# Performance work log

Measured on AMD Instinct MI355X. Metric: run time of the kernel, lower is better.

Reference implementation:

```python
import jax, jax.numpy as jnp
import numpy as np

EMBED = 1024
HEADS = 16
DEPTH = EMBED // HEADS
FFN_DIM = 4096
EPS = 1e-9


def layer_norm(x, g, b):
    mu = jnp.mean(x, axis=-1, keepdims=True)
    var = jnp.mean(jnp.square(x - mu), axis=-1, keepdims=True)
    return (x - mu) * jax.lax.rsqrt(var + EPS) * g + b


def setup_inputs() -> dict:
    key = jax.random.key(0)
    ks = jax.random.split(key, 16)
    B, S = 2, 2048
    s_e = 1.0 / np.sqrt(EMBED)
    s_f = 1.0 / np.sqrt(FFN_DIM)
    return {
        "x": jax.random.normal(ks[0], (B, S, EMBED), dtype=jnp.float32),
        "mask": jnp.zeros((B, 1, 1, S), dtype=jnp.float32),
        "wq_w": jax.random.normal(ks[1], (EMBED, EMBED), dtype=jnp.float32) * s_e,
        "wq_b": jnp.zeros((EMBED,), dtype=jnp.float32),
        "wk_w": jax.random.normal(ks[2], (EMBED, EMBED), dtype=jnp.float32) * s_e,
        "wk_b": jnp.zeros((EMBED,), dtype=jnp.float32),
        "wv_w": jax.random.normal(ks[3], (EMBED, EMBED), dtype=jnp.float32) * s_e,
        "wv_b": jnp.zeros((EMBED,), dtype=jnp.float32),
        "wo_w": jax.random.normal(ks[4], (EMBED, EMBED), dtype=jnp.float32) * s_e,
        "wo_b": jnp.zeros((EMBED,), dtype=jnp.float32),
        "f1_w": jax.random.normal(ks[5], (EMBED, FFN_DIM), dtype=jnp.float32) * s_e,
        "f1_b": jnp.zeros((FFN_DIM,), dtype=jnp.float32),
        "f2_w": jax.random.normal(ks[6], (FFN_DIM, EMBED), dtype=jnp.float32) * s_f,
        "f2_b": jnp.zeros((EMBED,), dtype=jnp.float32),
        "ln1_g": jnp.ones((EMBED,), dtype=jnp.float32),
        "ln1_b": jnp.zeros((EMBED,), dtype=jnp.float32),
        "ln2_g": jnp.ones((EMBED,), dtype=jnp.float32),
        "ln2_b": jnp.zeros((EMBED,), dtype=jnp.float32),
    }


def reference(x, mask, wq_w, wq_b, wk_w, wk_b, wv_w, wv_b, wo_w, wo_b,
              f1_w, f1_b, f2_w, f2_b, ln1_g, ln1_b, ln2_g, ln2_b):
    B, S, E = x.shape

    def split_heads(t):  # (B,S,E) -> (B,H,S,D)
        return t.reshape(B, S, HEADS, DEPTH).transpose(0, 2, 1, 3)

    q = split_heads(x @ wq_w + wq_b)
    k = split_heads(x @ wk_w + wk_b)
    v = split_heads(x @ wv_w + wv_b)

    logits = jnp.einsum("bhqd,bhkd->bhqk", q, k) / jnp.sqrt(jnp.float32(DEPTH))
    logits = logits + mask * -1e12  # mask broadcast (B,1,1,S)
    attn = jax.nn.softmax(logits, axis=-1)
    out = jnp.einsum("bhqk,bhkd->bhqd", attn, v)
    out = out.transpose(0, 2, 1, 3).reshape(B, S, E)
    out = out @ wo_w + wo_b

    # dropout is identity (is_train=False)
    h = layer_norm(out + x, ln1_g, ln1_b)
    f = jax.nn.relu(h @ f1_w + f1_b) @ f2_w + f2_b
    return layer_norm(f + h, ln2_g, ln2_b)
```

## Files before the change

kernel.cpp:

```cpp
#include <hip/hip_runtime.h>
#include <hip/hip_bf16.h>
#include <stdint.h>

typedef __hip_bfloat16 bf16;
typedef __attribute__((ext_vector_type(8))) short short8;
typedef __attribute__((ext_vector_type(4))) short short4v;
typedef __attribute__((ext_vector_type(4))) float floatx4;

#define E_DIM 1024
#define S_LEN 2048
#define NB    2
#define NH    16
#define HD    64
#define FFN   4096
#define MTOT  4096

__device__ __forceinline__ void gl_lds16(const void* g, void* l) {
  __builtin_amdgcn_global_load_lds(
      (__attribute__((address_space(1))) void*)(g),
      (__attribute__((address_space(3))) void*)(l), 16, 0, 0);
}

#define VMW(N)  do { asm volatile("s_waitcnt vmcnt(" #N ")" ::: "memory"); \
                     __builtin_amdgcn_sched_barrier(0); } while (0)
#define LGKM0   do { asm volatile("s_waitcnt lgkmcnt(0)" ::: "memory"); } while (0)
#define BARR    do { asm volatile("s_barrier" ::: "memory"); } while (0)

__device__ __forceinline__ int fswz_v(int row) { return row & 7; }
__device__ __forceinline__ int fswz_k(int row) {
  return ((row ^ (row >> 3)) & 3) | ((((row >> 3) ^ (row >> 4)) & 1) << 2);
}

__device__ __forceinline__ float bf16bits2float(short s) {
  union { unsigned u; float f; } c;
  c.u = ((unsigned)(unsigned short)s) << 16;
  return c.f;
}

__global__ __launch_bounds__(256)
void cvt_bf16(const float* __restrict__ in, bf16* __restrict__ out) {
  const size_t i = ((size_t)blockIdx.x * 256 + threadIdx.x) * 4;
  float4 v = *(const float4*)(in + i);
  out[i + 0] = __float2bfloat16(v.x);
  out[i + 1] = __float2bfloat16(v.y);
  out[i + 2] = __float2bfloat16(v.z);
  out[i + 3] = __float2bfloat16(v.w);
}

__global__ __launch_bounds__(256)
void transpose_all(const float* __restrict__ wq, const float* __restrict__ wk,
                   const float* __restrict__ wv, const float* __restrict__ wo,
                   const float* __restrict__ f1, const float* __restrict__ f2,
                   bf16* __restrict__ W3T, bf16* __restrict__ woT,
                   bf16* __restrict__ f1T, bf16* __restrict__ f2T) {
  const int z = blockIdx.z;
  const float* in;
  bf16* out;
  int inStride, outStride, rOff, cOff;
  if (z < 4) {
    in = (z == 0) ? wq : (z == 1) ? wk : (z == 2) ? wv : wo;
    out = (z < 3) ? (W3T + (size_t)z * 1024 * 1024) : woT;
    inStride = 1024; outStride = 1024; rOff = 0; cOff = 0;
  } else if (z < 8) {
    in = f1; out = f1T; inStride = 4096; outStride = 1024;
    rOff = 0; cOff = (z - 4) * 1024;
  } else {
    in = f2; out = f2T; inStride = 1024; outStride = 4096;
    rOff = (z - 8) * 1024; cOff = 0;
  }
  __shared__ float tile[32][33];
  const int tx = threadIdx.x & 31;
  const int ty = threadIdx.x >> 5;
  const int c0 = blockIdx.x * 32;
  const int r0 = blockIdx.y * 32;
#pragma unroll
  for (int j = 0; j < 32; j += 8)
    tile[ty + j][tx] =
        in[(size_t)(rOff + r0 + ty + j) * inStride + cOff + c0 + tx];
  __syncthreads();
#pragma unroll
  for (int j = 0; j < 32; j += 8)
    out[(size_t)(cOff + c0 + ty + j) * outStride + rOff + r0 + tx] =
        __float2bfloat16(tile[tx][ty + j]);
}

__global__ __launch_bounds__(256)
void prep_bias(const float* __restrict__ qb, const float* __restrict__ kb,
               const float* __restrict__ vb, float* __restrict__ out) {
  const int i = blockIdx.x * 256 + threadIdx.x;
  float v = (i < 1024) ? qb[i] * 0.125f
                       : ((i < 2048) ? kb[i - 1024] : vb[i - 2048]);
  out[i] = v;
}

__global__ __launch_bounds__(512, 2)
void gemm256(const bf16* __restrict__ A, const bf16* __restrict__ B,
             const float* __restrict__ bias, void* __restrict__ Cout,
             void* __restrict__ Cout2,
             int M, int N, int Kpart, int lda, int mode) {
  __shared__ alignas(16) bf16 sA[2][2][128 * 64];
  __shared__ alignas(16) bf16 sB[2][2][128 * 64];
  const int tid   = threadIdx.x;
  const int wave  = tid >> 6;
  const int lane  = tid & 63;
  const int row16 = lane & 15;
  const int quad  = lane >> 4;
  const int sw7   = row16 & 7;

  const int gx = gridDim.x;
  const int nwg = gx * gridDim.y;
  const int cpx = nwg >> 3;
  int id = blockIdx.y * gx + blockIdx.x;
  id = (id & 7) * cpx + (id >> 3);
  const int m0 = (id % gx) * 256;
  const int n0 = (id / gx) * 256;

  const int wm2 = wave >> 2;
  const int wn4 = wave & 3;
  const int wm  = wm2 * 128;
  const int wn  = wn4 * 64;
  const int hB  = wn4 >> 1;
  const int rbB = (wn4 & 1) * 64;
  const int koff = blockIdx.z * Kpart;
  const int NS = Kpart >> 6;

  floatx4 acc[8][4];
#pragma unroll
  for (int i = 0; i < 8; i++)
#pragma unroll
    for (int j = 0; j < 4; j++) {
      floatx4 z = {0.f, 0.f, 0.f, 0.f};
      acc[i][j] = z;
    }

  auto stage_half = [&](const bf16* G, int rowBase, int k0, bf16* dst) {
#pragma unroll
    for (int j = 0; j < 2; ++j) {
      const int r = wave * 16 + j * 8 + (lane >> 3);
      const int g = (lane & 7) ^ (r & 7);
      gl_lds16(G + (size_t)(rowBase + r) * lda + k0 + g * 8,
               dst + (wave * 16 + j * 8) * 64);
    }
  };

  short8 aF[8][2];
  short8 bF[4][2];
  const bf16* aH = nullptr;
  const bf16* bH = nullptr;

  auto read_aF = [&](int mi0) {
#pragma unroll
    for (int mi = 0; mi < 4; ++mi)
#pragma unroll
      for (int kk = 0; kk < 2; ++kk)
        aF[mi0 + mi][kk] = *(const short8*)(
            aH + ((mi0 + mi) * 16 + row16) * 64 + (((kk * 4 + quad) ^ sw7) << 3));
  };
  auto read_bF = [&](int ni0) {
#pragma unroll
    for (int ni = 0; ni < 2; ++ni)
#pragma unroll
      for (int kk = 0; kk < 2; ++kk)
        bF[ni0 + ni][kk] = *(const short8*)(
            bH + (rbB + (ni0 + ni) * 16 + row16) * 64 + (((kk * 4 + quad) ^ sw7) << 3));
  };
  auto qmf = [&](int mi0, int ni0) {
    __builtin_amdgcn_s_setprio(1);
#pragma unroll
    for (int mi = 0; mi < 4; ++mi)
#pragma unroll
      for (int ni = 0; ni < 2; ++ni)
#pragma unroll
        for (int kk = 0; kk < 2; ++kk)
          acc[mi0 + mi][ni0 + ni] = __builtin_amdgcn_mfma_f32_16x16x32_bf16(
              aF[mi0 + mi][kk], bF[ni0 + ni][kk], acc[mi0 + mi][ni0 + ni], 0, 0, 0);
    __builtin_amdgcn_s_setprio(0);
  };

  stage_half(A, m0,       koff,      &sA[0][0][0]);
  stage_half(A, m0 + 128, koff,      &sA[0][1][0]);
  stage_half(B, n0,       koff,      &sB[0][0][0]);
  stage_half(B, n0 + 128, koff,      &sB[0][1][0]);
  stage_half(A, m0,       koff + 64, &sA[1][0][0]);
  stage_half(A, m0 + 128, koff + 64, &sA[1][1][0]);

  for (int s = 0; s < NS; ++s) {
    const int b = s & 1;
    aH = &sA[b][wm2][0];
    bH = &sB[b][hB][0];
    if (s + 1 < NS) VMW(4); else VMW(0);
    BARR;
    if (s + 1 < NS) {
      const int kn1 = koff + (s + 1) * 64;
      stage_half(B, n0,       kn1, &sB[b ^ 1][0][0]);
      stage_half(B, n0 + 128, kn1, &sB[b ^ 1][1][0]);
    }
    read_aF(0);
    read_bF(0);
    read_aF(4);
    qmf(0, 0);
    qmf(4, 0);
    LGKM0;
    BARR;
    if (s + 2 < NS) {
      const int kn2 = koff + (s + 2) * 64;
      stage_half(A, m0,       kn2, &sA[b][0][0]);
      stage_half(A, m0 + 128, kn2, &sA[b][1][0]);
    }
    read_bF(2);
    qmf(0, 2);
    qmf(4, 2);
  }

  float bval[4] = {0.f, 0.f, 0.f, 0.f};
  if (mode != 0) {
#pragma unroll
    for (int ni = 0; ni < 4; ni++) bval[ni] = bias[n0 + wn + ni * 16 + row16];
  }

#pragma unroll
  for (int mi = 0; mi < 8; mi++) {
#pragma unroll
    for (int ni = 0; ni < 4; ni++) {
      const int col = n0 + wn + ni * 16 + row16;
      if (mode == 0) {
        float* co = (float*)((blockIdx.z < 2) ? Cout : Cout2) +
                    (size_t)(blockIdx.z & 1) * M * N;
#pragma unroll
        for (int r = 0; r < 4; r++) {
          const int row = m0 + wm + mi * 16 + quad * 4 + r;
          co[(size_t)row * N + col] = acc[mi][ni][r];
        }
      } else if (mode == 1) {
#pragma unroll
        for (int r = 0; r < 4; r++) {
          const int row = m0 + wm + mi * 16 + quad * 4 + r;
          float v = acc[mi][ni][r] + bval[ni];
          v = v > 0.f ? v : 0.f;
          ((bf16*)Cout)[(size_t)row * N + col] = __float2bfloat16(v);
        }
      } else {
        const int mat = col >> 10;
        const int c10 = col & 1023;
        const int hh = c10 >> 6, dd = c10 & 63;
        const float scl = (mat == 0) ? 0.125f : 1.0f;
        bf16* qout = (bf16*)Cout;
        const int rbase = m0 + wm + mi * 16 + quad * 4;
        const int b2 = rbase >> 11, ss = rbase & 2047;
        const size_t bh = (size_t)b2 * NH + hh;
        if (mat == 2) {
          bf16* vt = qout + (1 << 23);
          short4v pv;
#pragma unroll
          for (int r = 0; r < 4; r++) {
            bf16 t = __float2bfloat16(acc[mi][ni][r] + bval[ni]);
            pv[r] = *(short*)&t;
          }
          *(short4v*)(vt + (bh * HD + dd) * S_LEN + ss) = pv;
        } else {
          bf16* o = (mat == 1) ? (qout + (1 << 22)) : qout;
#pragma unroll
          for (int r = 0; r < 4; r++) {
            float v = acc[mi][ni][r] * scl + bval[ni];
            o[(bh * S_LEN + ss + r) * HD + dd] = __float2bfloat16(v);
          }
        }
      }
    }
  }
}

__global__ __launch_bounds__(256, 4)
void flash_attn(const bf16* __restrict__ Q, const bf16* __restrict__ K,
                const bf16* __restrict__ Vt, const float* __restrict__ mask,
                bf16* __restrict__ Out) {
  __shared__ alignas(16) bf16 sK[2][64 * 64];
  __shared__ alignas(16) bf16 sV[2][64 * 64];
  __shared__ alignas(16) float sM[S_LEN];

  const int tid   = threadIdx.x;
  const int wave  = tid >> 6;
  const int lane  = tid & 63;
  const int row16 = lane & 15;
  const int quad  = lane >> 4;
  const int bh = blockIdx.y;
  const int b = bh >> 4, h = bh & 15;
  const int q0 = blockIdx.x * 64;
  const int qg = q0 + wave * 16 + row16;

  const bf16* qp = Q + ((size_t)bh * S_LEN + qg) * HD;
  short8 qf0 = *(const short8*)(qp + quad * 8);
  short8 qf1 = *(const short8*)(qp + 32 + quad * 8);

  for (int i = tid; i < S_LEN / 4; i += 256) {
    float4 mv = ((const float4*)(mask + (size_t)b * S_LEN))[i];
    float4 w = {-1e12f * mv.x, -1e12f * mv.y, -1e12f * mv.z, -1e12f * mv.w};
    ((float4*)sM)[i] = w;
  }
  LGKM0;

  float lsum = 0.f;
  floatx4 ov[4];
#pragma unroll
  for (int i = 0; i < 4; i++) { floatx4 z = {0.f,0.f,0.f,0.f}; ov[i] = z; }

  const bf16* Kbase = K + (size_t)bh * S_LEN * HD;
  const bf16* Vbase = Vt + (size_t)bh * HD * S_LEN;
  const int NT = S_LEN / 64;

  auto stage = [&](int kt) {
    const bf16* Kg = Kbase + (size_t)kt * 64 * HD;
    const bf16* Vg = Vbase + kt * 64;
    bf16* dK = sK[kt & 1];
    bf16* dV = sV[kt & 1];
#pragma unroll
    for (int j = 0; j < 2; ++j) {
      const int ch = wave * 2 + j;
      const int row = ch * 8 + (lane >> 3);
      const int sc_ = lane & 7;
      gl_lds16(Kg + row * 64 + ((sc_ ^ fswz_k(row)) * 8), dK + ch * 512);
      gl_lds16(Vg + (size_t)row * S_LEN + ((sc_ ^ fswz_v(row)) * 8), dV + ch * 512);
    }
  };

  stage(0);

  for (int kt = 0; kt < NT; ++kt) {
    if (kt + 1 < NT) {
      stage(kt + 1);
      VMW(4);
    } else {
      VMW(0);
    }
    BARR;

    const bf16* Kb = sK[kt & 1];
    const bf16* Vb = sV[kt & 1];

    floatx4 sc[4];
#pragma unroll
    for (int mi = 0; mi < 4; mi++) {
      const int row = ((row16 >> 2) << 3) + (row16 & 3) + ((mi & 1) << 2) + ((mi >> 1) << 5);
      const int fk = fswz_k(row);
      short8 kf0 = *(const short8*)(Kb + row * 64 + ((quad ^ fk) << 3));
      short8 kf1 = *(const short8*)(Kb + row * 64 + (((4 + quad) ^ fk) << 3));
      floatx4 z = {0.f, 0.f, 0.f, 0.f};
      z = __builtin_amdgcn_mfma_f32_16x16x32_bf16(kf0, qf0, z, 0, 0, 0);
      sc[mi] = __builtin_amdgcn_mfma_f32_16x16x32_bf16(kf1, qf1, z, 0, 0, 0);
    }

#pragma unroll
    for (int mi = 0; mi < 4; mi++) {
      float4 mv = *(const float4*)(sM + kt * 64 + (quad << 3) + ((mi & 1) << 2) + ((mi >> 1) << 5));
      sc[mi][0] = __expf(sc[mi][0] + mv.x);
      sc[mi][1] = __expf(sc[mi][1] + mv.y);
      sc[mi][2] = __expf(sc[mi][2] + mv.z);
      sc[mi][3] = __expf(sc[mi][3] + mv.w);
      lsum += sc[mi][0] + sc[mi][1] + sc[mi][2] + sc[mi][3];
    }

    short8 pf[2];
#pragma unroll
    for (int ks = 0; ks < 2; ks++)
#pragma unroll
      for (int jp = 0; jp < 4; jp++) {
        const int mi = 2 * ks + (jp >> 1);
        const int r0 = (jp & 1) * 2;
        bf16 p0 = __float2bfloat16(sc[mi][r0]);
        bf16 p1 = __float2bfloat16(sc[mi][r0 + 1]);
        pf[ks][2 * jp]     = *(short*)&p0;
        pf[ks][2 * jp + 1] = *(short*)&p1;
      }

#pragma unroll
    for (int mi = 0; mi < 4; mi++) {
      const int row = mi * 16 + row16;
      const int fv = fswz_v(row);
      short8 v0 = *(const short8*)(Vb + row * 64 + ((quad ^ fv) << 3));
      short8 v1 = *(const short8*)(Vb + row * 64 + (((4 + quad) ^ fv) << 3));
      ov[mi] = __builtin_amdgcn_mfma_f32_16x16x32_bf16(v0, pf[0], ov[mi], 0, 0, 0);
      ov[mi] = __builtin_amdgcn_mfma_f32_16x16x32_bf16(v1, pf[1], ov[mi], 0, 0, 0);
    }
    BARR;
  }

  lsum += __shfl_xor(lsum, 16);
  lsum += __shfl_xor(lsum, 32);
  const float inv = 1.0f / lsum;
#pragma unroll
  for (int mi = 0; mi < 4; mi++) {
    short4v pv;
#pragma unroll
    for (int r = 0; r < 4; r++) {
      bf16 t = __float2bfloat16(ov[mi][r] * inv);
      pv[r] = *(short*)&t;
    }
    *(short4v*)(Out + ((size_t)(b * S_LEN + qg)) * E_DIM + h * HD + mi * 16 + quad * 4) = pv;
  }
}

__global__ __launch_bounds__(256)
void ln_reduce(const float* __restrict__ p0, const float* __restrict__ p1,
               const float* __restrict__ p2, const float* __restrict__ p3,
               const float* __restrict__ resf, const bf16* __restrict__ resb,
               const float* __restrict__ bias, const float* __restrict__ g,
               const float* __restrict__ be, float* __restrict__ outf,
               bf16* __restrict__ outb) {
  const int row = blockIdx.x;
  const int tid = threadIdx.x;
  const size_t base = (size_t)row * 1024;
  const int c = tid * 4;
  float4 a = *(const float4*)(p0 + base + c);
  float4 bq = *(const float4*)(p1 + base + c);
  float4 xv;
  xv.x = a.x + bq.x;
  xv.y = a.y + bq.y;
  xv.z = a.z + bq.z;
  xv.w = a.w + bq.w;
  if (p2) {
    float4 a2 = *(const float4*)(p2 + base + c);
    float4 a3 = *(const float4*)(p3 + base + c);
    xv.x += a2.x + a3.x;
    xv.y += a2.y + a3.y;
    xv.z += a2.z + a3.z;
    xv.w += a2.w + a3.w;
  }
  float4 rv;
  if (resf) {
    rv = *(const float4*)(resf + base + c);
  } else {
    short4v rb = *(const short4v*)((const short*)resb + base + c);
    rv.x = bf16bits2float(rb[0]);
    rv.y = bf16bits2float(rb[1]);
    rv.z = bf16bits2float(rb[2]);
    rv.w = bf16bits2float(rb[3]);
  }
  float4 bi = *(const float4*)(bias + c);
  xv.x += rv.x + bi.x;
  xv.y += rv.y + bi.y;
  xv.z += rv.z + bi.z;
  xv.w += rv.w + bi.w;
  float s  = xv.x + xv.y + xv.z + xv.w;
  float s2 = xv.x * xv.x + xv.y * xv.y + xv.z * xv.z + xv.w * xv.w;
#pragma unroll
  for (int d = 1; d < 64; d <<= 1) {
    s  += __shfl_xor(s, d);
    s2 += __shfl_xor(s2, d);
  }
  __shared__ float red[2][4];
  const int wave = tid >> 6;
  if ((tid & 63) == 0) { red[0][wave] = s; red[1][wave] = s2; }
  __syncthreads();
  s  = red[0][0] + red[0][1] + red[0][2] + red[0][3];
  s2 = red[1][0] + red[1][1] + red[1][2] + red[1][3];
  const float mu  = s * (1.0f / 1024.0f);
  const float var = s2 * (1.0f / 1024.0f) - mu * mu;
  const float rs  = rsqrtf(var + 1e-9f);
  float4 gg = *(const float4*)(g + c);
  float4 bb = *(const float4*)(be + c);
  float4 y;
  y.x = (xv.x - mu) * rs * gg.x + bb.x;
  y.y = (xv.y - mu) * rs * gg.y + bb.y;
  y.z = (xv.z - mu) * rs * gg.z + bb.z;
  y.w = (xv.w - mu) * rs * gg.w + bb.w;
  if (outf) *(float4*)(outf + base + c) = y;
  if (outb) {
    bf16* o = outb + base + c;
    o[0] = __float2bfloat16(y.x);
    o[1] = __float2bfloat16(y.y);
    o[2] = __float2bfloat16(y.z);
    o[3] = __float2bfloat16(y.w);
  }
}

extern "C" void kernel_launch(void* const* d_in, const int* in_sizes, int n_in,
                              void* d_out, int out_size, void* d_ws,
                              size_t ws_size, hipStream_t stream) {
  const float* x    = (const float*)d_in[0];
  const float* mask = (const float*)d_in[1];
  const float* wq_w = (const float*)d_in[2];
  const float* wq_b = (const float*)d_in[3];
  const float* wk_w = (const float*)d_in[4];
  const float* wk_b = (const float*)d_in[5];
  const float* wv_w = (const float*)d_in[6];
  const float* wv_b = (const float*)d_in[7];
  const float* wo_w = (const float*)d_in[8];
  const float* wo_b = (const float*)d_in[9];
  const float* f1_w = (const float*)d_in[10];
  const float* f1_b = (const float*)d_in[11];
  const float* f2_w = (const float*)d_in[12];
  const float* f2_b = (const float*)d_in[13];
  const float* ln1_g = (const float*)d_in[14];
  const float* ln1_b = (const float*)d_in[15];
  const float* ln2_g = (const float*)d_in[16];
  const float* ln2_b = (const float*)d_in[17];
  float* out = (float*)d_out;

  char* ws = (char*)d_ws;
  const size_t MB = 1u << 20;
  bf16*  xbf   = (bf16*)(ws + 0 * MB);
  bf16*  W3T   = (bf16*)(ws + 8 * MB);
  bf16*  woT   = (bf16*)(ws + 14 * MB);
  float* bqkv  = (float*)(ws + 16 * MB);
  bf16*  Qb    = (bf16*)(ws + 17 * MB);
  bf16*  attnb = (bf16*)(ws + 0 * MB);
  bf16*  ffn1  = (bf16*)(ws + 17 * MB);
  bf16*  f1T   = (bf16*)(ws + 49 * MB);
  bf16*  f2T   = (bf16*)(ws + 57 * MB);
  float* P01   = (float*)(ws + 65 * MB);
  bf16*  hbf   = (bf16*)(ws + 97 * MB);
  float* P23   = (float*)(ws + 105 * MB);
  const size_t PS = (size_t)MTOT * E_DIM;

  const int KS = (ws_size >= (size_t)137 * MB) ? 4 : 2;
  const float* p2 = (KS == 4) ? P23 : nullptr;
  const float* p3 = (KS == 4) ? P23 + PS : nullptr;

  cvt_bf16<<<4096, 256, 0, stream>>>(x, xbf);
  transpose_all<<<dim3(32, 32, 12), 256, 0, stream>>>(
      wq_w, wk_w, wv_w, wo_w, f1_w, f2_w, W3T, woT, f1T, f2T);
  prep_bias<<<12, 256, 0, stream>>>(wq_b, wk_b, wv_b, bqkv);

  gemm256<<<dim3(16, 12, 1), 512, 0, stream>>>(
      xbf, W3T, bqkv, Qb, nullptr, MTOT, 3 * E_DIM, E_DIM, E_DIM, 2);

  flash_attn<<<dim3(S_LEN / 64, NB * NH), 256, 0, stream>>>(
      Qb, Qb + (1 << 22), Qb + (1 << 23), mask, attnb);

  gemm256<<<dim3(16, 4, KS), 512, 0, stream>>>(
      attnb, woT, nullptr, P01, P23, MTOT, E_DIM, E_DIM / KS, E_DIM, 0);

  ln_reduce<<<MTOT, 256, 0, stream>>>(P01, P01 + PS, p2, p3, x, nullptr,
                                      wo_b, ln1_g, ln1_b, nullptr, hbf);

  gemm256<<<dim3(16, 16, 1), 512, 0, stream>>>(
      hbf, f1T, f1_b, ffn1, nullptr, MTOT, FFN, E_DIM, E_DIM, 1);

  gemm256<<<dim3(16, 4, KS), 512, 0, stream>>>(
      ffn1, f2T, nullptr, P01, P23, MTOT, E_DIM, FFN / KS, FFN, 0);

  ln_reduce<<<MTOT, 256, 0, stream>>>(P01, P01 + PS, p2, p3, nullptr, hbf,
                                      f2_b, ln2_g, ln2_b, out, nullptr);
}
```

Before: 377.4 us.

## Fold log2e into Q scale, use exp2, compute row sums via MFMA

Folds log2(e) into the query scale and the mask constant so the softmax can use the raw v_exp_f32 (exp2) instruction in place of __expf. It replaces the per-lane scalar row-sum accumulation and cross-lane shuffles with two MFMAs against a ones vector, so the sum comes out of the matrix unit. The sum now uses bf16-rounded probabilities, consistent with what feeds P·V. Separately, the GEMM main loop reorders its fragment reads and MFMA calls to issue all B reads first and overlap the A reads with compute.

Measured after the change: 376.0 us. Within noise of the previous version (-0.4%).

```diff
diff --git a/kernel.cpp b/kernel.cpp
--- a/kernel.cpp
+++ b/kernel.cpp
@@ -15,6 +15,9 @@
 #define FFN   4096
 #define MTOT  4096
 
+#define QSCALE 0.18033688011112042f
+#define MSCALE -1.4426950408889634e12f
+
 __device__ __forceinline__ void gl_lds16(const void* g, void* l) {
   __builtin_amdgcn_global_load_lds(
       (__attribute__((address_space(1))) void*)(g),
@@ -25,6 +28,12 @@
                      __builtin_amdgcn_sched_barrier(0); } while (0)
 #define LGKM0   do { asm volatile("s_waitcnt lgkmcnt(0)" ::: "memory"); } while (0)
 #define BARR    do { asm volatile("s_barrier" ::: "memory"); } while (0)
+
+__device__ __forceinline__ float exp2_fast(float x) {
+  float r;
+  asm("v_exp_f32 %0, %1" : "=v"(r) : "v"(x));
+  return r;
+}
 
 __device__ __forceinline__ int fswz_v(int row) { return row & 7; }
 __device__ __forceinline__ int fswz_k(int row) {
@@ -88,7 +97,7 @@
 void prep_bias(const float* __restrict__ qb, const float* __restrict__ kb,
                const float* __restrict__ vb, float* __restrict__ out) {
   const int i = blockIdx.x * 256 + threadIdx.x;
-  float v = (i < 1024) ? qb[i] * 0.125f
+  float v = (i < 1024) ? qb[i] * QSCALE
                        : ((i < 2048) ? kb[i - 1024] : vb[i - 2048]);
   out[i] = v;
 }
@@ -195,11 +204,12 @@
       stage_half(B, n0,       kn1, &sB[b ^ 1][0][0]);
       stage_half(B, n0 + 128, kn1, &sB[b ^ 1][1][0]);
     }
+    read_bF(0);
+    read_bF(2);
     read_aF(0);
-    read_bF(0);
+    qmf(0, 0);
+    qmf(0, 2);
     read_aF(4);
-    qmf(0, 0);
-    qmf(4, 0);
     LGKM0;
     BARR;
     if (s + 2 < NS) {
@@ -207,8 +217,7 @@
       stage_half(A, m0,       kn2, &sA[b][0][0]);
       stage_half(A, m0 + 128, kn2, &sA[b][1][0]);
     }
-    read_bF(2);
-    qmf(0, 2);
+    qmf(4, 0);
     qmf(4, 2);
   }
 
@@ -243,7 +252,7 @@
         const int mat = col >> 10;
         const int c10 = col & 1023;
         const int hh = c10 >> 6, dd = c10 & 63;
-        const float scl = (mat == 0) ? 0.125f : 1.0f;
+        const float scl = (mat == 0) ? QSCALE : 1.0f;
         bf16* qout = (bf16*)Cout;
         const int rbase = m0 + wm + mi * 16 + quad * 4;
         const int b2 = rbase >> 11, ss = rbase & 2047;
@@ -294,12 +303,16 @@
 
   for (int i = tid; i < S_LEN / 4; i += 256) {
     float4 mv = ((const float4*)(mask + (size_t)b * S_LEN))[i];
-    float4 w = {-1e12f * mv.x, -1e12f * mv.y, -1e12f * mv.z, -1e12f * mv.w};
+    float4 w = {MSCALE * mv.x, MSCALE * mv.y, MSCALE * mv.z, MSCALE * mv.w};
     ((float4*)sM)[i] = w;
   }
   LGKM0;
 
-  float lsum = 0.f;
+  short8 ones;
+#pragma unroll
+  for (int j = 0; j < 8; j++) ones[j] = (short)0x3F80;
+
+  floatx4 lacc = {0.f, 0.f, 0.f, 0.f};
   floatx4 ov[4];
 #pragma unroll
   for (int i = 0; i < 4; i++) { floatx4 z = {0.f,0.f,0.f,0.f}; ov[i] = z; }
@@ -352,11 +365,10 @@
 #pragma unroll
     for (int mi = 0; mi < 4; mi++) {
       float4 mv = *(const float4*)(sM + kt * 64 + (quad << 3) + ((mi & 1) << 2) + ((mi >> 1) << 5));
-      sc[mi][0] = __expf(sc[mi][0] + mv.x);
-      sc[mi][1] = __expf(sc[mi][1] + mv.y);
-      sc[mi][2] = __expf(sc[mi][2] + mv.z);
-      sc[mi][3] = __expf(sc[mi][3] + mv.w);
-      lsum += sc[mi][0] + sc[mi][1] + sc[mi][2] + sc[mi][3];
+      sc[mi][0] = exp2_fast(sc[mi][0] + mv.x);
+      sc[mi][1] = exp2_fast(sc[mi][1] + mv.y);
+      sc[mi][2] = exp2_fast(sc[mi][2] + mv.z);
+      sc[mi][3] = exp2_fast(sc[mi][3] + mv.w);
     }
 
     short8 pf[2];
@@ -372,6 +384,9 @@
         pf[ks][2 * jp + 1] = *(short*)&p1;
       }
 
+    lacc = __builtin_amdgcn_mfma_f32_16x16x32_bf16(ones, pf[0], lacc, 0, 0, 0);
+    lacc = __builtin_amdgcn_mfma_f32_16x16x32_bf16(ones, pf[1], lacc, 0, 0, 0);
+
 #pragma unroll
     for (int mi = 0; mi < 4; mi++) {
       const int row = mi * 16 + row16;
@@ -384,9 +399,7 @@
     BARR;
   }
 
-  lsum += __shfl_xor(lsum, 16);
-  lsum += __shfl_xor(lsum, 32);
-  const float inv = 1.0f / lsum;
+  const float inv = 1.0f / lacc[0];
 #pragma unroll
   for (int mi = 0; mi < 4; mi++) {
     short4v pv;
```
